# Kernel optimization log

Measured on AMD Instinct MI355X. Metric: run time of the kernel, lower is better.

Reference implementation:

```python
import jax, jax.numpy as jnp
import numpy as np

HEADS = 16
KV_HEADS = 8
HEAD_DIM = 128
ROPE_BASE = 10000.0
RMS_EPS = 1e-5


def rmsnorm(x, w, eps=RMS_EPS):
    x = jnp.clip(x.astype(jnp.float32), -100.0, 100.0)
    var = jnp.clip(jnp.mean(x * x, axis=-1, keepdims=True), eps, None)
    x = x * jax.lax.rsqrt(var + eps)
    x = jnp.clip(x, -10.0, 10.0)
    return w * x


def activation_quant(x):
    x = jnp.clip(x, -50.0, 50.0)
    max_val = jnp.clip(jnp.max(jnp.abs(x), axis=-1, keepdims=True), 0.0001, None)
    scale = 127.0 / max_val
    return jnp.clip(jnp.round(x * scale), -128.0, 127.0) / scale


def weight_quant(w):
    scale = jnp.clip(jnp.mean(jnp.abs(w)), 1e-8, None)
    e = jnp.mean(w)
    return jnp.sign(w - e) * scale


def bitlinear(x, w, norm_w):
    xn = rmsnorm(x, norm_w)
    xq = xn + jax.lax.stop_gradient(activation_quant(xn) - xn)
    wq = w + jax.lax.stop_gradient(weight_quant(w) - w)
    return xq @ wq.T


def rope_tables(seq_len, dim):
    inv_freq = 1.0 / (ROPE_BASE ** (jnp.arange(0, dim, 2, dtype=jnp.float32) / dim))
    freqs = jnp.outer(jnp.arange(seq_len, dtype=jnp.float32), inv_freq)  # [S, dim/2]
    emb = jnp.concatenate([freqs, freqs], axis=-1)  # [S, dim]
    return jnp.cos(emb), jnp.sin(emb)


def rotate_half(x):
    x1, x2 = jnp.split(x, 2, axis=-1)
    return jnp.concatenate([-x2, x1], axis=-1)


def attention_forward(hidden_states, attention_mask, wq, wk, wv, wo, nq, nk, nv, no):
    B, S, H = hidden_states.shape
    q = bitlinear(hidden_states, wq, nq)  # [B,S,nh*hd]
    k = bitlinear(hidden_states, wk, nk)  # [B,S,nkv*hd]
    v = bitlinear(hidden_states, wv, nv)

    q = q.reshape(B, S, HEADS, HEAD_DIM).transpose(0, 2, 1, 3)       # [B,nh,S,hd]
    k = k.reshape(B, S, KV_HEADS, HEAD_DIM).transpose(0, 2, 1, 3)    # [B,nkv,S,hd]
    v = v.reshape(B, S, KV_HEADS, HEAD_DIM).transpose(0, 2, 1, 3)

    cos, sin = rope_tables(S, HEAD_DIM)
    cos = cos[None, None]  # [1,1,S,hd]
    sin = sin[None, None]
    q = q * cos + rotate_half(q) * sin
    k = k * cos + rotate_half(k) * sin

    groups = HEADS // KV_HEADS
    k_exp = jnp.repeat(k, groups, axis=1)  # [B,nh,S,hd]
    v_exp = jnp.repeat(v, groups, axis=1)

    scale = 1.0 / jnp.sqrt(jnp.float32(HEAD_DIM))
    scores = jnp.einsum('bhqd,bhkd->bhqk', q, k_exp) * scale
    scores = scores + attention_mask
    attn = jax.nn.softmax(scores, axis=-1)
    out = jnp.einsum('bhqk,bhkd->bhqd', attn, v_exp)
    out = out.transpose(0, 2, 1, 3).reshape(B, S, HEADS * HEAD_DIM)
    return bitlinear(out, wo, no)


def setup_inputs() -> dict:
    key = jax.random.key(0)
    ks = jax.random.split(key, 6)
    B, S, H = 2, 2048, 2048
    KVH = KV_HEADS * HEAD_DIM
    std = 0.02 / np.sqrt(H)
    return {
        'hidden_states': jax.random.normal(ks[0], (B, S, H), jnp.float32),
        'attention_mask': jnp.zeros((1, 1, S, S), jnp.float32),
        'wq': jax.random.normal(ks[1], (H, H), jnp.float32) * std,
        'wk': jax.random.normal(ks[2], (KVH, H), jnp.float32) * std,
        'wv': jax.random.normal(ks[3], (KVH, H), jnp.float32) * std,
        'wo': jax.random.normal(ks[4], (H, H), jnp.float32) * std,
        'nq': jnp.ones((H,), jnp.float32),
        'nk': jnp.ones((H,), jnp.float32),
        'nv': jnp.ones((H,), jnp.float32),
        'no': jnp.ones((H,), jnp.float32),
    }


def reference(hidden_states, attention_mask, wq, wk, wv, wo, nq, nk, nv, no):
    return attention_forward(hidden_states, attention_mask, wq, wk, wv, wo, nq, nk, nv, no)
```

## Files before the change

### kernel.cpp

```cpp
#include <hip/hip_runtime.h>


#define DI __device__ __forceinline__

using bf16   = __bf16;
using bf16x4 = __attribute__((ext_vector_type(4))) __bf16;
using bf16x8 = __attribute__((ext_vector_type(8))) __bf16;
using f32x4  = __attribute__((ext_vector_type(4))) float;

DI void gl_lds16(void* lds, const void* g) {
  __builtin_amdgcn_global_load_lds((const __attribute__((address_space(1))) void*)g,
                                   (__attribute__((address_space(3))) void*)lds, 16, 0, 0);
}
DI float clampf(float x, float lo, float hi) { return fminf(fmaxf(x, lo), hi); }

DI float block_sum(float v, float* red, int lane, int w) {
#pragma unroll
  for (int o = 32; o > 0; o >>= 1) v += __shfl_xor(v, o, 64);
  __syncthreads();
  if (lane == 0) red[w] = v;
  __syncthreads();
  return red[0] + red[1] + red[2] + red[3];
}

__global__ void wstats_kernel(const float* wq, const float* wk, const float* wv,
                              const float* wo, float* stats) {
  __shared__ float red[4], red2[4];
  int t = threadIdx.x, lane = t & 63, w = t >> 6;
  int m = blockIdx.y;
  const float* src; int n4;
  if (m == 0)      { src = wq; n4 = 1048576; }
  else if (m == 1) { src = wk; n4 = 524288;  }
  else if (m == 2) { src = wv; n4 = 524288;  }
  else             { src = wo; n4 = 1048576; }
  float s = 0.f, sa = 0.f;
  for (int i = blockIdx.x * 256 + t; i < n4; i += 256 * 256) {
    float4 v = ((const float4*)src)[i];
    s  += v.x + v.y + v.z + v.w;
    sa += fabsf(v.x) + fabsf(v.y) + fabsf(v.z) + fabsf(v.w);
  }
#pragma unroll
  for (int o = 32; o > 0; o >>= 1) { s += __shfl_xor(s, o, 64); sa += __shfl_xor(sa, o, 64); }
  if (lane == 0) { red[w] = s; red2[w] = sa; }
  __syncthreads();
  if (t == 0) {
    atomicAdd(&stats[2 * m],     red[0] + red[1] + red[2] + red[3]);
    atomicAdd(&stats[2 * m + 1], red2[0] + red2[1] + red2[2] + red2[3]);
  }
}

__global__ void wsign_kernel(const float* wq, const float* wk, const float* wv, const float* wo,
                             ushort* sq, ushort* sk, ushort* sv, ushort* so,
                             const float* stats) {
  int m = blockIdx.y;
  const float* src; ushort* dst; int n4; float cinv;
  if (m == 0)      { src = wq; dst = sq; n4 = 1048576; cinv = 1.f / 4194304.f; }
  else if (m == 1) { src = wk; dst = sk; n4 = 524288;  cinv = 1.f / 2097152.f; }
  else if (m == 2) { src = wv; dst = sv; n4 = 524288;  cinv = 1.f / 2097152.f; }
  else             { src = wo; dst = so; n4 = 1048576; cinv = 1.f / 4194304.f; }
  float e = stats[2 * m] * cinv;
  for (int i = blockIdx.x * 256 + threadIdx.x; i < n4; i += 1024 * 256) {
    float4 v = ((const float4*)src)[i];
    ushort4 o;
    o.x = v.x > e ? 0x3F80 : (v.x < e ? 0xBF80 : 0);
    o.y = v.y > e ? 0x3F80 : (v.y < e ? 0xBF80 : 0);
    o.z = v.z > e ? 0x3F80 : (v.z < e ? 0xBF80 : 0);
    o.w = v.w > e ? 0x3F80 : (v.w < e ? 0xBF80 : 0);
    ((ushort4*)dst)[i] = o;
  }
}

__global__ void ropetab_kernel(float* ct, float* st) {
  int s = blockIdx.x, j = threadIdx.x;
  float invf = powf(10000.f, -(float)j * (1.f / 64.f));
  float a = (float)s * invf;
  ct[s * 64 + j] = cosf(a);
  st[s * 64 + j] = sinf(a);
}

template <int NW>
__launch_bounds__(256)
__global__ void rqnorm_kernel(const float* __restrict__ x,
                              const float* __restrict__ w0, const float* __restrict__ w1,
                              const float* __restrict__ w2,
                              bf16* a0, bf16* a1, bf16* a2,
                              float* r0, float* r1, float* r2) {
  __shared__ float red[4];
  __shared__ float redm[4][NW];
  int t = threadIdx.x, lane = t & 63, w = t >> 6;
  int row = blockIdx.x;
  const float* xr = x + (size_t)row * 2048;
  float4 u0 = ((const float4*)xr)[t * 2], u1 = ((const float4*)xr)[t * 2 + 1];
  float xs[8] = {u0.x, u0.y, u0.z, u0.w, u1.x, u1.y, u1.z, u1.w};
  float ss = 0.f;
#pragma unroll
  for (int e = 0; e < 8; ++e) { xs[e] = clampf(xs[e], -100.f, 100.f); ss += xs[e] * xs[e]; }
  float tot = block_sum(ss, red, lane, w);
  float var = fmaxf(tot * (1.f / 2048.f), 1e-5f);
  float inv = 1.f / sqrtf(var + 1e-5f);
#pragma unroll
  for (int e = 0; e < 8; ++e) xs[e] = clampf(xs[e] * inv, -10.f, 10.f);

  float y[NW][8], am[NW];
#pragma unroll
  for (int m = 0; m < NW; ++m) {
    const float* wt = (m == 0) ? w0 : (m == 1) ? w1 : w2;
    float4 b0 = ((const float4*)wt)[t * 2], b1 = ((const float4*)wt)[t * 2 + 1];
    float wv[8] = {b0.x, b0.y, b0.z, b0.w, b1.x, b1.y, b1.z, b1.w};
    am[m] = 0.f;
#pragma unroll
    for (int e = 0; e < 8; ++e) {
      y[m][e] = clampf(wv[e] * xs[e], -50.f, 50.f);
      am[m] = fmaxf(am[m], fabsf(y[m][e]));
    }
  }
#pragma unroll
  for (int o = 32; o > 0; o >>= 1)
#pragma unroll
    for (int m = 0; m < NW; ++m) am[m] = fmaxf(am[m], __shfl_xor(am[m], o, 64));
  if (lane == 0)
#pragma unroll
    for (int m = 0; m < NW; ++m) redm[w][m] = am[m];
  __syncthreads();
#pragma unroll
  for (int m = 0; m < NW; ++m) {
    bf16* a = (m == 0) ? a0 : (m == 1) ? a1 : a2;
    float* r = (m == 0) ? r0 : (m == 1) ? r1 : r2;
    float mx = fmaxf(fmaxf(redm[0][m], redm[1][m]), fmaxf(redm[2][m], redm[3][m]));
    float maxval = fmaxf(mx, 1e-4f);
    float sc = 127.f / maxval;
    bf16x8 q;
#pragma unroll
    for (int e = 0; e < 8; ++e)
      q[e] = (bf16)clampf(rintf(y[m][e] * sc), -128.f, 127.f);
    *(bf16x8*)(a + (size_t)row * 2048 + t * 8) = q;
    if (t == 0) r[row] = maxval * (1.f / 127.f);
  }
}

DI void mm_core(const bf16* __restrict__ Ag0, const bf16* __restrict__ Bg0,
                bf16* As, bf16* Bs, int w, int lane, f32x4 acc[2][8]) {
  int l15 = lane & 15, quad = lane >> 4;
  int srow = w * 8 + (lane >> 3);
  int sc_p = (lane & 7) * 8;
  int sc_g = ((lane & 7) ^ (lane >> 3)) * 8;
  const bf16* Ag = Ag0 + (size_t)srow * 2048 + sc_g;
  const bf16* Bg = Bg0 + (size_t)srow * 2048 + sc_g;
  bf16* Al = As + srow * 64 + sc_p;
  bf16* Bl = Bs + srow * 64 + sc_p;
  auto stage = [&](int buf, int kt) {
    size_t kb = (size_t)kt * 64;
    int lo = buf * 8192;
#pragma unroll
    for (int i = 0; i < 4; ++i) {
      gl_lds16(Al + lo + i * 32 * 64, Ag + (size_t)i * 32 * 2048 + kb);
      gl_lds16(Bl + lo + i * 32 * 64, Bg + (size_t)i * 32 * 2048 + kb);
    }
  };
  stage(0, 0);
  for (int kt = 0; kt < 32; ++kt) {
    int cur = kt & 1;
    __syncthreads();
    if (kt < 31) stage(cur ^ 1, kt + 1);
    const bf16* Ac = As + cur * 8192;
    const bf16* Bc = Bs + cur * 8192;
#pragma unroll
    for (int kc = 0; kc < 2; ++kc) {
      bf16x8 af[2], bfr[8];
#pragma unroll
      for (int mt = 0; mt < 2; ++mt)
        af[mt] = *(const bf16x8*)(Ac + (w * 32 + mt * 16 + l15) * 64 +
                                  (((kc * 4 + quad) ^ (l15 & 7)) * 8));
#pragma unroll
      for (int nt = 0; nt < 8; ++nt)
        bfr[nt] = *(const bf16x8*)(Bc + (nt * 16 + l15) * 64 +
                                   (((kc * 4 + quad) ^ (l15 & 7)) * 8));
#pragma unroll
      for (int mt = 0; mt < 2; ++mt)
#pragma unroll
        for (int nt = 0; nt < 8; ++nt)
          acc[mt][nt] = __builtin_amdgcn_mfma_f32_16x16x32_bf16(af[mt], bfr[nt], acc[mt][nt], 0, 0, 0);
    }
  }
}

__launch_bounds__(256, 2)
__global__ void qkv_gemm(const bf16* __restrict__ Aq, const bf16* __restrict__ Ak,
                         const bf16* __restrict__ Av, const bf16* __restrict__ Ball,
                         const float* __restrict__ rq, const float* __restrict__ rk,
                         const float* __restrict__ rv, const float* __restrict__ stats,
                         bf16* __restrict__ qr, bf16* __restrict__ kr,
                         bf16* __restrict__ vt,
                         const float* __restrict__ ct, const float* __restrict__ st) {
  __shared__ bf16 As[2 * 128 * 64];
  __shared__ bf16 Bs[2 * 128 * 64];
  int t = threadIdx.x, w = t >> 6, lane = t & 63;
  int l15 = lane & 15, quad = lane >> 4;
  int bid = blockIdx.y * 32 + blockIdx.x;
  bid = (bid & 7) * 128 + (bid >> 3);
  int x = bid & 31, m0 = (bid >> 5) * 128;
  const bf16* A; const float* rs; float sw; int brow0;
  if (x < 16)      { A = Aq; rs = rq; sw = stats[1] * (1.f / 4194304.f); brow0 = x * 128; }
  else if (x < 24) { A = Ak; rs = rk; sw = stats[3] * (1.f / 2097152.f); brow0 = 2048 + (x - 16) * 128; }
  else             { A = Av; rs = rv; sw = stats[5] * (1.f / 2097152.f); brow0 = 3072 + (x - 24) * 128; }
  sw = fmaxf(sw, 1e-8f);
  f32x4 acc[2][8] = {};
  mm_core(A + (size_t)m0 * 2048, Ball + (size_t)brow0 * 2048, As, Bs, w, lane, acc);

  if (x < 24) {
    constexpr float QROPE = 0.08838834764831845f * 1.4426950408889634f;
    float qmul = (x < 16) ? QROPE : 1.f;
    bf16* outb = (x < 16) ? qr : kr;
    int h = (x < 16) ? x : x - 16;
    int nh = (x < 16) ? 16 : 8;
#pragma unroll
    for (int mt = 0; mt < 2; ++mt)
#pragma unroll
      for (int r = 0; r < 4; ++r) {
        int row = m0 + w * 32 + mt * 16 + quad * 4 + r;
        float rsc = rs[row] * sw * qmul;
        int s = row & 2047, b = row >> 11;
        size_t base = ((size_t)(b * nh + h) * 2048 + s) * 128;
#pragma unroll
        for (int nt = 0; nt < 4; ++nt) {
          int d = nt * 16 + l15;
          float x1 = acc[mt][nt][r] * rsc;
          float x2 = acc[mt][nt + 4][r] * rsc;
          float c = ct[s * 64 + d], sn = st[s * 64 + d];
          outb[base + d]      = (bf16)(x1 * c - x2 * sn);
          outb[base + d + 64] = (bf16)(x2 * c + x1 * sn);
        }
      }
  } else {
    int kvh = x - 24;
    bf16* tile = As;
    __syncthreads();
#pragma unroll
    for (int mt = 0; mt < 2; ++mt)
#pragma unroll
      for (int r = 0; r < 4; ++r) {
        int tok = w * 32 + mt * 16 + quad * 4 + r;
        float rsc = rs[m0 + tok] * sw;
#pragma unroll
        for (int nt = 0; nt < 8; ++nt) {
          int f = nt * 16 + l15;
          tile[f * 128 + (tok ^ ((f & 7) << 3))] = (bf16)(acc[mt][nt][r] * rsc);
        }
      }
    __syncthreads();
    int f = t >> 1, tok0 = (t & 1) * 64;
    int btok = m0 >> 11, s0 = m0 & 2047;
    bf16* dst = vt + ((size_t)(btok * 8 + kvh) * 128 + f) * 2048 + s0 + tok0;
    int sxor = (f & 7) << 3;
#pragma unroll
    for (int j = 0; j < 8; ++j) {
      bf16x8 vv = *(const bf16x8*)(tile + f * 128 + ((tok0 + j * 8) ^ sxor));
      *(bf16x8*)(dst + j * 8) = vv;
    }
  }
}

__launch_bounds__(256, 2)
__global__ void gemm_o(const bf16* __restrict__ A, const bf16* __restrict__ Bw,
                       const float* __restrict__ rs, const float* __restrict__ stats,
                       float* __restrict__ out) {
  __shared__ bf16 As[2 * 128 * 64];
  __shared__ bf16 Bs[2 * 128 * 64];
  int t = threadIdx.x, w = t >> 6, lane = t & 63;
  int l15 = lane & 15, quad = lane >> 4;
  int bid = blockIdx.y * 16 + blockIdx.x;
  bid = (bid & 7) * 64 + (bid >> 3);
  int n0 = (bid & 15) * 128, m0 = (bid >> 4) * 128;
  f32x4 acc[2][8] = {};
  mm_core(A + (size_t)m0 * 2048, Bw + (size_t)n0 * 2048, As, Bs, w, lane, acc);
  float sw = fmaxf(stats[7] * (1.f / 4194304.f), 1e-8f);
#pragma unroll
  for (int mt = 0; mt < 2; ++mt)
#pragma unroll
    for (int r = 0; r < 4; ++r) {
      int row = m0 + w * 32 + mt * 16 + quad * 4 + r;
      float rsc = rs[row] * sw;
#pragma unroll
      for (int nt = 0; nt < 8; ++nt)
        out[(size_t)row * 2048 + n0 + nt * 16 + l15] = acc[mt][nt][r] * rsc;
    }
}

__launch_bounds__(512, 4)
__global__ void attn_kernel(const bf16* __restrict__ Q, const bf16* __restrict__ Kc,
                            const bf16* __restrict__ Vt, const float* __restrict__ mask,
                            float* __restrict__ Oout) {
  constexpr float L2E  = 1.4426950408889634f;
  constexpr float DTHR = 8.f * L2E;
  __shared__ bf16 Ks[2][64 * 128];
  __shared__ bf16 Vs[2][128 * 64];
  __shared__ bf16 Ps[128 * 64];
  int t = threadIdx.x, w = t >> 6, lane = t & 63;
  int l15 = lane & 15, quad = lane >> 4;
  int bh = blockIdx.y, b = bh >> 4, h = bh & 15, kvh = h >> 1;
  int q0 = blockIdx.x * 128;
  const bf16* Qb = Q + (size_t)(b * 16 + h) * 2048 * 128;
  const bf16* Kb = Kc + (size_t)(b * 8 + kvh) * 2048 * 128;
  const bf16* Vb = Vt + (size_t)(b * 8 + kvh) * 128 * 2048;

  int qloc = w * 16 + l15;
  int qg = q0 + qloc;

  bf16x8 qf[4];
#pragma unroll
  for (int kc = 0; kc < 4; ++kc)
    qf[kc] = *(const bf16x8*)(Qb + (size_t)qg * 128 + kc * 32 + quad * 8);

  f32x4 Oa[8] = {};
  float mrow = -1e30f, lrow = 0.f;

  auto stage = [&](int buf, int kt) {
    int kk0 = kt * 64;
#pragma unroll
    for (int i = 0; i < 2; ++i) {
      int c = t + i * 512;
      int kr = c >> 4, c16 = c & 15;
      gl_lds16(&Ks[buf][c * 8],
               Kb + (size_t)(kk0 + kr) * 128 + ((c16 ^ (kr & 15)) * 8));
    }
#pragma unroll
    for (int i = 0; i < 2; ++i) {
      int c = t + i * 512;
      int vr = c >> 3, c8 = c & 7;
      gl_lds16(&Vs[buf][c * 8],
               Vb + (size_t)vr * 2048 + kk0 + ((c8 ^ (vr & 7)) * 8));
    }
  };

  stage(0, 0);

  f32x4 mv[4];
#pragma unroll
  for (int k2 = 0; k2 < 4; ++k2)
    mv[k2] = *(const f32x4*)(mask + (size_t)qg * 2048 + k2 * 16 + quad * 4);

  for (int kt = 0; kt < 32; ++kt) {
    int cur = kt & 1;
    __syncthreads();
    if (kt < 31) stage(cur ^ 1, kt + 1);

    f32x4 Sacc[4] = {};
    __builtin_amdgcn_s_setprio(1);
#pragma unroll
    for (int kc = 0; kc < 4; ++kc) {
      bf16x8 kf[4];
#pragma unroll
      for (int k2 = 0; k2 < 4; ++k2)
        kf[k2] = *(const bf16x8*)(&Ks[cur][(k2 * 16 + l15) * 128 + (((kc * 4 + quad) ^ l15) * 8)]);
#pragma unroll
      for (int k2 = 0; k2 < 4; ++k2)
        Sacc[k2] = __builtin_amdgcn_mfma_f32_16x16x32_bf16(kf[k2], qf[kc], Sacc[k2], 0, 0, 0);
    }
    __builtin_amdgcn_s_setprio(0);

#pragma unroll
    for (int k2 = 0; k2 < 4; ++k2)
#pragma unroll
      for (int r = 0; r < 4; ++r)
        Sacc[k2][r] = fmaf(mv[k2][r], L2E, Sacc[k2][r]);
    f32x4 vm;
#pragma unroll
    for (int r = 0; r < 4; ++r)
      vm[r] = fmaxf(fmaxf(Sacc[0][r], Sacc[1][r]), fmaxf(Sacc[2][r], Sacc[3][r]));
    float mx = fmaxf(fmaxf(vm[0], vm[1]), fmaxf(vm[2], vm[3]));
    mx = fmaxf(mx, __shfl_xor(mx, 16, 64));
    mx = fmaxf(mx, __shfl_xor(mx, 32, 64));
    if (!__all(mx <= mrow + DTHR)) {
      float mnew = fmaxf(mrow, mx);
      float alpha = exp2f(mrow - mnew);
      mrow = mnew;
      lrow *= alpha;
#pragma unroll
      for (int dt = 0; dt < 8; ++dt) Oa[dt] *= alpha;
    }
    f32x4 vs = {0.f, 0.f, 0.f, 0.f};
#pragma unroll
    for (int k2 = 0; k2 < 4; ++k2) {
      bf16x4 pk;
#pragma unroll
      for (int r = 0; r < 4; ++r) {
        float p = exp2f(Sacc[k2][r] - mrow);
        vs[r] += p;
        pk[r] = (bf16)p;
      }
      int c = k2 * 2 + (quad >> 1);
      *(bf16x4*)(&Ps[qloc * 64 + ((c ^ (qloc & 7)) * 8) + (quad & 1) * 4]) = pk;
    }
    float rsum = (vs[0] + vs[1]) + (vs[2] + vs[3]);
    rsum += __shfl_xor(rsum, 16, 64);
    rsum += __shfl_xor(rsum, 32, 64);
    lrow += rsum;

    if (kt < 31) {
      int kk1 = (kt + 1) * 64;
#pragma unroll
      for (int k2 = 0; k2 < 4; ++k2)
        mv[k2] = *(const f32x4*)(mask + (size_t)qg * 2048 + kk1 + k2 * 16 + quad * 4);
    }

    __builtin_amdgcn_s_setprio(1);
#pragma unroll
    for (int kc = 0; kc < 2; ++kc) {
      bf16x8 pf = *(const bf16x8*)(&Ps[qloc * 64 + (((kc * 4 + quad) ^ (l15 & 7)) * 8)]);
#pragma unroll
      for (int dt = 0; dt < 8; ++dt) {
        bf16x8 vf = *(const bf16x8*)(&Vs[cur][(dt * 16 + l15) * 64 +
                                              (((kc * 4 + quad) ^ (l15 & 7)) * 8)]);
        Oa[dt] = __builtin_amdgcn_mfma_f32_16x16x32_bf16(vf, pf, Oa[dt], 0, 0, 0);
      }
    }
    __builtin_amdgcn_s_setprio(0);
  }

  float inv = 1.f / lrow;
  int token = b * 2048 + qg;
#pragma unroll
  for (int dt = 0; dt < 8; ++dt) {
    f32x4 o = Oa[dt] * inv;
    *(f32x4*)(Oout + (size_t)token * 2048 + h * 128 + dt * 16 + quad * 4) = o;
  }
}

extern "C" void kernel_launch(void* const* d_in, const int* in_sizes, int n_in,
                              void* d_out, int out_size, void* d_ws, size_t ws_size,
                              hipStream_t stream) {
  const float* hidden = (const float*)d_in[0];
  const float* mask   = (const float*)d_in[1];
  const float* wq = (const float*)d_in[2];
  const float* wk = (const float*)d_in[3];
  const float* wv = (const float*)d_in[4];
  const float* wo = (const float*)d_in[5];
  const float* nq = (const float*)d_in[6];
  const float* nk = (const float*)d_in[7];
  const float* nv = (const float*)d_in[8];
  const float* no = (const float*)d_in[9];
  float* out = (float*)d_out;
  char* ws = (char*)d_ws;

  constexpr size_t O_STATS = 0;
  constexpr size_t O_CT    = 256;
  constexpr size_t O_ST    = O_CT + 524288;
  constexpr size_t O_SQ    = O_ST + 524288;
  constexpr size_t O_SK    = O_SQ + 8388608;
  constexpr size_t O_SV    = O_SK + 4194304;
  constexpr size_t O_SO    = O_SV + 4194304;
  constexpr size_t O_RSQ   = O_SO + 8388608;
  constexpr size_t O_RSK   = O_RSQ + 16384;
  constexpr size_t O_RSV   = O_RSK + 16384;
  constexpr size_t O_RSO   = O_RSV + 16384;
  constexpr size_t O_AQQ   = O_RSO + 16384;
  constexpr size_t O_AQK   = O_AQQ + 16777216;
  constexpr size_t O_AQV   = O_AQK + 16777216;
  constexpr size_t O_QR    = O_AQV + 16777216;
  constexpr size_t O_KR    = O_QR + 16777216;
  constexpr size_t O_VT    = O_KR + 8388608;
  constexpr size_t O_ATTN  = O_AQQ;
  constexpr size_t O_AQO   = O_AQV;

  float* stats = (float*)(ws + O_STATS);
  float* ct = (float*)(ws + O_CT);
  float* st = (float*)(ws + O_ST);

  (void)hipMemsetAsync(ws + O_STATS, 0, 256, stream);

  wstats_kernel<<<dim3(256, 4), 256, 0, stream>>>(wq, wk, wv, wo, stats);
  wsign_kernel<<<dim3(1024, 4), 256, 0, stream>>>(wq, wk, wv, wo,
      (ushort*)(ws + O_SQ), (ushort*)(ws + O_SK), (ushort*)(ws + O_SV), (ushort*)(ws + O_SO), stats);
  ropetab_kernel<<<dim3(2048), 64, 0, stream>>>(ct, st);

  rqnorm_kernel<3><<<dim3(4096), 256, 0, stream>>>(hidden, nq, nk, nv,
      (bf16*)(ws + O_AQQ), (bf16*)(ws + O_AQK), (bf16*)(ws + O_AQV),
      (float*)(ws + O_RSQ), (float*)(ws + O_RSK), (float*)(ws + O_RSV));

  qkv_gemm<<<dim3(32, 32), 256, 0, stream>>>(
      (const bf16*)(ws + O_AQQ), (const bf16*)(ws + O_AQK), (const bf16*)(ws + O_AQV),
      (const bf16*)(ws + O_SQ),
      (const float*)(ws + O_RSQ), (const float*)(ws + O_RSK), (const float*)(ws + O_RSV),
      stats, (bf16*)(ws + O_QR), (bf16*)(ws + O_KR), (bf16*)(ws + O_VT), ct, st);

  attn_kernel<<<dim3(16, 32), 512, 0, stream>>>(
      (const bf16*)(ws + O_QR), (const bf16*)(ws + O_KR), (const bf16*)(ws + O_VT),
      mask, (float*)(ws + O_ATTN));

  rqnorm_kernel<1><<<dim3(4096), 256, 0, stream>>>((const float*)(ws + O_ATTN), no, no, no,
      (bf16*)(ws + O_AQO), (bf16*)(ws + O_AQO), (bf16*)(ws + O_AQO),
      (float*)(ws + O_RSO), (float*)(ws + O_RSO), (float*)(ws + O_RSO));

  gemm_o<<<dim3(16, 32), 256, 0, stream>>>(
      (const bf16*)(ws + O_AQO), (const bf16*)(ws + O_SO), (float*)(ws + O_RSO), stats, out);

  (void)in_sizes; (void)n_in; (void)out_size; (void)ws_size;
}
```

Measured before the change: 423.8 us.

## Enlarge GEMM tiles to 256 with 8-wave pipelined core and separate V transpose

Replaces the 128x128 GEMM core with a templated 512-thread pipeline using 256x256 tiles for QKV and 128x256 for the output projection. It prefetches two stages ahead with explicit vmcnt waits, barriers and setprio around the MFMAs. The aim is more operand reuse per loaded byte and better overlap of loads with compute. V is now written as fp32 linear output and transposed to bf16 by a new kernel, which adds an extra pass and a scratch buffer. The larger LDS use (128KB for QKV) may cut occupancy, and 256 blocks may underfill the GPU.

New measurement: 420.5 us. No clear change (-0.8%).

```diff
diff --git a/kernel.cpp b/kernel.cpp
--- a/kernel.cpp
+++ b/kernel.cpp
@@ -13,6 +13,12 @@
                                    (__attribute__((address_space(3))) void*)lds, 16, 0, 0);
 }
 DI float clampf(float x, float lo, float hi) { return fminf(fmaxf(x, lo), hi); }
+
+template <int N> DI void wait_vm() {
+  if constexpr (N == 8)      asm volatile("s_waitcnt vmcnt(8)" ::: "memory");
+  else if constexpr (N == 6) asm volatile("s_waitcnt vmcnt(6)" ::: "memory");
+  else                       asm volatile("s_waitcnt vmcnt(0)" ::: "memory");
+}
 
 DI float block_sum(float v, float* red, int lane, int w) {
 #pragma unroll
@@ -138,152 +144,182 @@
   }
 }
 
-DI void mm_core(const bf16* __restrict__ Ag0, const bf16* __restrict__ Bg0,
-                bf16* As, bf16* Bs, int w, int lane, f32x4 acc[2][8]) {
-  int l15 = lane & 15, quad = lane >> 4;
-  int srow = w * 8 + (lane >> 3);
-  int sc_p = (lane & 7) * 8;
-  int sc_g = ((lane & 7) ^ (lane >> 3)) * 8;
-  const bf16* Ag = Ag0 + (size_t)srow * 2048 + sc_g;
-  const bf16* Bg = Bg0 + (size_t)srow * 2048 + sc_g;
-  bf16* Al = As + srow * 64 + sc_p;
-  bf16* Bl = Bs + srow * 64 + sc_p;
+template <int BM, int BN>
+DI void mm_pipe(const bf16* __restrict__ Ag0, const bf16* __restrict__ Bg0,
+                bf16* As, bf16* Bs, int t, f32x4 (&acc)[BM / 64][BN / 32]) {
+  constexpr int MR = BM / 64, NR = BN / 32;
+  constexpr int AL = BM / 64, BL = BN / 64;
+  constexpr int NT = 32;
+  int lane = t & 63, l15 = lane & 15, quad = lane >> 4;
+  int wv = t >> 6, wm = wv >> 1, wn = wv & 1;
+  const bf16* agp[AL]; const bf16* bgp[BL];
+#pragma unroll
+  for (int i = 0; i < AL; ++i) {
+    int c = t + i * 512, row = c >> 3, c8 = c & 7;
+    agp[i] = Ag0 + (size_t)row * 2048 + (c8 ^ (row & 7)) * 8;
+  }
+#pragma unroll
+  for (int i = 0; i < BL; ++i) {
+    int c = t + i * 512, row = c >> 3, c8 = c & 7;
+    bgp[i] = Bg0 + (size_t)row * 2048 + (c8 ^ (row & 7)) * 8;
+  }
   auto stage = [&](int buf, int kt) {
-    size_t kb = (size_t)kt * 64;
-    int lo = buf * 8192;
-#pragma unroll
-    for (int i = 0; i < 4; ++i) {
-      gl_lds16(Al + lo + i * 32 * 64, Ag + (size_t)i * 32 * 2048 + kb);
-      gl_lds16(Bl + lo + i * 32 * 64, Bg + (size_t)i * 32 * 2048 + kb);
-    }
+    int kb = kt * 64;
+#pragma unroll
+    for (int i = 0; i < AL; ++i)
+      gl_lds16(As + buf * (BM * 64) + (t + i * 512) * 8, agp[i] + kb);
+#pragma unroll
+    for (int i = 0; i < BL; ++i)
+      gl_lds16(Bs + buf * (BN * 64) + (t + i * 512) * 8, bgp[i] + kb);
   };
   stage(0, 0);
-  for (int kt = 0; kt < 32; ++kt) {
+  stage(1, 1);
+  int arow = wm * (BM / 4) + l15;
+  int brow = wn * (BN / 2) + l15;
+  int rsw = l15 & 7;
+  for (int kt = 0; kt < NT; ++kt) {
     int cur = kt & 1;
-    __syncthreads();
-    if (kt < 31) stage(cur ^ 1, kt + 1);
-    const bf16* Ac = As + cur * 8192;
-    const bf16* Bc = Bs + cur * 8192;
+    if (kt == NT - 1) wait_vm<0>(); else wait_vm<AL + BL>();
+    __builtin_amdgcn_sched_barrier(0);
+    __builtin_amdgcn_s_barrier();
+    __builtin_amdgcn_sched_barrier(0);
+    const bf16* Ac = As + cur * (BM * 64);
+    const bf16* Bc = Bs + cur * (BN * 64);
+    __builtin_amdgcn_s_setprio(1);
 #pragma unroll
     for (int kc = 0; kc < 2; ++kc) {
-      bf16x8 af[2], bfr[8];
-#pragma unroll
-      for (int mt = 0; mt < 2; ++mt)
-        af[mt] = *(const bf16x8*)(Ac + (w * 32 + mt * 16 + l15) * 64 +
-                                  (((kc * 4 + quad) ^ (l15 & 7)) * 8));
-#pragma unroll
-      for (int nt = 0; nt < 8; ++nt)
-        bfr[nt] = *(const bf16x8*)(Bc + (nt * 16 + l15) * 64 +
-                                   (((kc * 4 + quad) ^ (l15 & 7)) * 8));
-#pragma unroll
-      for (int mt = 0; mt < 2; ++mt)
-#pragma unroll
-        for (int nt = 0; nt < 8; ++nt)
-          acc[mt][nt] = __builtin_amdgcn_mfma_f32_16x16x32_bf16(af[mt], bfr[nt], acc[mt][nt], 0, 0, 0);
-    }
-  }
-}
-
-__launch_bounds__(256, 2)
+      int co = ((kc * 4 + quad) ^ rsw) * 8;
+      bf16x8 af[MR], bfr[NR];
+#pragma unroll
+      for (int m = 0; m < MR; ++m)
+        af[m] = *(const bf16x8*)(Ac + (arow + m * 16) * 64 + co);
+#pragma unroll
+      for (int n = 0; n < NR; ++n)
+        bfr[n] = *(const bf16x8*)(Bc + (brow + n * 16) * 64 + co);
+#pragma unroll
+      for (int m = 0; m < MR; ++m)
+#pragma unroll
+        for (int n = 0; n < NR; ++n)
+          acc[m][n] = __builtin_amdgcn_mfma_f32_16x16x32_bf16(af[m], bfr[n], acc[m][n], 0, 0, 0);
+    }
+    __builtin_amdgcn_s_setprio(0);
+    __builtin_amdgcn_sched_barrier(0);
+    __builtin_amdgcn_s_barrier();
+    __builtin_amdgcn_sched_barrier(0);
+    if (kt + 2 < NT) stage(cur, kt + 2);
+  }
+}
+
+__launch_bounds__(512, 2)
 __global__ void qkv_gemm(const bf16* __restrict__ Aq, const bf16* __restrict__ Ak,
                          const bf16* __restrict__ Av, const bf16* __restrict__ Ball,
                          const float* __restrict__ rq, const float* __restrict__ rk,
                          const float* __restrict__ rv, const float* __restrict__ stats,
                          bf16* __restrict__ qr, bf16* __restrict__ kr,
-                         bf16* __restrict__ vt,
+                         float* __restrict__ vlin,
                          const float* __restrict__ ct, const float* __restrict__ st) {
-  __shared__ bf16 As[2 * 128 * 64];
-  __shared__ bf16 Bs[2 * 128 * 64];
-  int t = threadIdx.x, w = t >> 6, lane = t & 63;
-  int l15 = lane & 15, quad = lane >> 4;
-  int bid = blockIdx.y * 32 + blockIdx.x;
-  bid = (bid & 7) * 128 + (bid >> 3);
-  int x = bid & 31, m0 = (bid >> 5) * 128;
-  const bf16* A; const float* rs; float sw; int brow0;
-  if (x < 16)      { A = Aq; rs = rq; sw = stats[1] * (1.f / 4194304.f); brow0 = x * 128; }
-  else if (x < 24) { A = Ak; rs = rk; sw = stats[3] * (1.f / 2097152.f); brow0 = 2048 + (x - 16) * 128; }
-  else             { A = Av; rs = rv; sw = stats[5] * (1.f / 2097152.f); brow0 = 3072 + (x - 24) * 128; }
+  __shared__ bf16 As[2 * 256 * 64];
+  __shared__ bf16 Bs[2 * 256 * 64];
+  int t = threadIdx.x;
+  int bid = blockIdx.x;
+  int swz = (bid & 7) * 32 + (bid >> 3);
+  int x = swz >> 4, mt = swz & 15;
+  int m0 = mt * 256;
+  const bf16* A; const float* rs; float sw;
+  if (x < 8)       { A = Aq; rs = rq; sw = stats[1] * (1.f / 4194304.f); }
+  else if (x < 12) { A = Ak; rs = rk; sw = stats[3] * (1.f / 2097152.f); }
+  else             { A = Av; rs = rv; sw = stats[5] * (1.f / 2097152.f); }
   sw = fmaxf(sw, 1e-8f);
-  f32x4 acc[2][8] = {};
-  mm_core(A + (size_t)m0 * 2048, Ball + (size_t)brow0 * 2048, As, Bs, w, lane, acc);
-
-  if (x < 24) {
+  f32x4 acc[4][8] = {};
+  mm_pipe<256, 256>(A + (size_t)m0 * 2048, Ball + (size_t)(x * 256) * 2048, As, Bs, t, acc);
+
+  int lane = t & 63, l15 = lane & 15, quad = lane >> 4;
+  int wv = t >> 6, wm = wv >> 1, wn = wv & 1;
+  if (x < 12) {
     constexpr float QROPE = 0.08838834764831845f * 1.4426950408889634f;
-    float qmul = (x < 16) ? QROPE : 1.f;
-    bf16* outb = (x < 16) ? qr : kr;
-    int h = (x < 16) ? x : x - 16;
-    int nh = (x < 16) ? 16 : 8;
-#pragma unroll
-    for (int mt = 0; mt < 2; ++mt)
+    float qmul = (x < 8) ? QROPE : 1.f;
+    bf16* outb = (x < 8) ? qr : kr;
+    int h = (x < 8) ? (x * 2 + wn) : ((x - 8) * 2 + wn);
+    int nh = (x < 8) ? 16 : 8;
+#pragma unroll
+    for (int m = 0; m < 4; ++m)
 #pragma unroll
       for (int r = 0; r < 4; ++r) {
-        int row = m0 + w * 32 + mt * 16 + quad * 4 + r;
+        int row = m0 + wm * 64 + m * 16 + quad * 4 + r;
         float rsc = rs[row] * sw * qmul;
         int s = row & 2047, b = row >> 11;
         size_t base = ((size_t)(b * nh + h) * 2048 + s) * 128;
 #pragma unroll
-        for (int nt = 0; nt < 4; ++nt) {
-          int d = nt * 16 + l15;
-          float x1 = acc[mt][nt][r] * rsc;
-          float x2 = acc[mt][nt + 4][r] * rsc;
+        for (int n = 0; n < 4; ++n) {
+          int d = n * 16 + l15;
+          float x1 = acc[m][n][r] * rsc;
+          float x2 = acc[m][n + 4][r] * rsc;
           float c = ct[s * 64 + d], sn = st[s * 64 + d];
           outb[base + d]      = (bf16)(x1 * c - x2 * sn);
           outb[base + d + 64] = (bf16)(x2 * c + x1 * sn);
         }
       }
   } else {
-    int kvh = x - 24;
-    bf16* tile = As;
-    __syncthreads();
-#pragma unroll
-    for (int mt = 0; mt < 2; ++mt)
+    int n0 = (x - 12) * 256 + wn * 128;
+#pragma unroll
+    for (int m = 0; m < 4; ++m)
 #pragma unroll
       for (int r = 0; r < 4; ++r) {
-        int tok = w * 32 + mt * 16 + quad * 4 + r;
-        float rsc = rs[m0 + tok] * sw;
-#pragma unroll
-        for (int nt = 0; nt < 8; ++nt) {
-          int f = nt * 16 + l15;
-          tile[f * 128 + (tok ^ ((f & 7) << 3))] = (bf16)(acc[mt][nt][r] * rsc);
-        }
+        int row = m0 + wm * 64 + m * 16 + quad * 4 + r;
+        float rsc = rs[row] * sw;
+#pragma unroll
+        for (int n = 0; n < 8; ++n)
+          vlin[(size_t)row * 1024 + n0 + n * 16 + l15] = acc[m][n][r] * rsc;
       }
-    __syncthreads();
-    int f = t >> 1, tok0 = (t & 1) * 64;
-    int btok = m0 >> 11, s0 = m0 & 2047;
-    bf16* dst = vt + ((size_t)(btok * 8 + kvh) * 128 + f) * 2048 + s0 + tok0;
-    int sxor = (f & 7) << 3;
-#pragma unroll
-    for (int j = 0; j < 8; ++j) {
-      bf16x8 vv = *(const bf16x8*)(tile + f * 128 + ((tok0 + j * 8) ^ sxor));
-      *(bf16x8*)(dst + j * 8) = vv;
-    }
-  }
-}
-
-__launch_bounds__(256, 2)
+  }
+}
+
+__launch_bounds__(512, 2)
 __global__ void gemm_o(const bf16* __restrict__ A, const bf16* __restrict__ Bw,
                        const float* __restrict__ rs, const float* __restrict__ stats,
                        float* __restrict__ out) {
   __shared__ bf16 As[2 * 128 * 64];
-  __shared__ bf16 Bs[2 * 128 * 64];
-  int t = threadIdx.x, w = t >> 6, lane = t & 63;
-  int l15 = lane & 15, quad = lane >> 4;
-  int bid = blockIdx.y * 16 + blockIdx.x;
-  bid = (bid & 7) * 64 + (bid >> 3);
-  int n0 = (bid & 15) * 128, m0 = (bid >> 4) * 128;
+  __shared__ bf16 Bs[2 * 256 * 64];
+  int t = threadIdx.x;
+  int bid = blockIdx.x;
+  int swz = (bid & 7) * 32 + (bid >> 3);
+  int x = swz & 7, mt = swz >> 3;
+  int m0 = mt * 128, n0 = x * 256;
   f32x4 acc[2][8] = {};
-  mm_core(A + (size_t)m0 * 2048, Bw + (size_t)n0 * 2048, As, Bs, w, lane, acc);
+  mm_pipe<128, 256>(A + (size_t)m0 * 2048, Bw + (size_t)n0 * 2048, As, Bs, t, acc);
   float sw = fmaxf(stats[7] * (1.f / 4194304.f), 1e-8f);
-#pragma unroll
-  for (int mt = 0; mt < 2; ++mt)
+  int lane = t & 63, l15 = lane & 15, quad = lane >> 4;
+  int wv = t >> 6, wm = wv >> 1, wn = wv & 1;
+#pragma unroll
+  for (int m = 0; m < 2; ++m)
 #pragma unroll
     for (int r = 0; r < 4; ++r) {
-      int row = m0 + w * 32 + mt * 16 + quad * 4 + r;
+      int row = m0 + wm * 32 + m * 16 + quad * 4 + r;
       float rsc = rs[row] * sw;
 #pragma unroll
-      for (int nt = 0; nt < 8; ++nt)
-        out[(size_t)row * 2048 + n0 + nt * 16 + l15] = acc[mt][nt][r] * rsc;
-    }
+      for (int n = 0; n < 8; ++n)
+        out[(size_t)row * 2048 + n0 + wn * 128 + n * 16 + l15] = acc[m][n][r] * rsc;
+    }
+}
+
+__global__ void vtrans_kernel(const float* __restrict__ v_lin, bf16* __restrict__ v_t) {
+  __shared__ float tile[64][65];
+  int t = threadIdx.x, c = t & 63, rq = t >> 6;
+  int ct0 = blockIdx.x * 64, tt0 = blockIdx.y * 64;
+#pragma unroll
+  for (int i = 0; i < 16; ++i) {
+    int r = rq * 16 + i;
+    tile[r][c] = v_lin[(size_t)(tt0 + r) * 1024 + ct0 + c];
+  }
+  __syncthreads();
+  int token = tt0 + c;
+  int b = token >> 11, s = token & 2047;
+#pragma unroll
+  for (int i = 0; i < 16; ++i) {
+    int cg = ct0 + rq * 16 + i;
+    int kvh = cg >> 7, d = cg & 127;
+    v_t[((size_t)(b * 8 + kvh) * 128 + d) * 2048 + s] = (bf16)tile[c][rq * 16 + i];
+  }
 }
 
 __launch_bounds__(512, 4)
@@ -459,6 +495,7 @@
   constexpr size_t O_QR    = O_AQV + 16777216;
   constexpr size_t O_KR    = O_QR + 16777216;
   constexpr size_t O_VT    = O_KR + 8388608;
+  constexpr size_t O_VLIN2 = O_VT + 8388608;
   constexpr size_t O_ATTN  = O_AQQ;
   constexpr size_t O_AQO   = O_AQV;
 
@@ -477,11 +514,13 @@
       (bf16*)(ws + O_AQQ), (bf16*)(ws + O_AQK), (bf16*)(ws + O_AQV),
       (float*)(ws + O_RSQ), (float*)(ws + O_RSK), (float*)(ws + O_RSV));
 
-  qkv_gemm<<<dim3(32, 32), 256, 0, stream>>>(
+  qkv_gemm<<<dim3(256), 512, 0, stream>>>(
       (const bf16*)(ws + O_AQQ), (const bf16*)(ws + O_AQK), (const bf16*)(ws + O_AQV),
       (const bf16*)(ws + O_SQ),
       (const float*)(ws + O_RSQ), (const float*)(ws + O_RSK), (const float*)(ws + O_RSV),
-      stats, (bf16*)(ws + O_QR), (bf16*)(ws + O_KR), (bf16*)(ws + O_VT), ct, st);
+      stats, (bf16*)(ws + O_QR), (bf16*)(ws + O_KR), (float*)(ws + O_VLIN2), ct, st);
+
+  vtrans_kernel<<<dim3(16, 64), 256, 0, stream>>>((const float*)(ws + O_VLIN2), (bf16*)(ws + O_VT));
 
   attn_kernel<<<dim3(16, 32), 512, 0, stream>>>(
       (const bf16*)(ws + O_QR), (const bf16*)(ws + O_KR), (const bf16*)(ws + O_VT),
@@ -491,7 +530,7 @@
       (bf16*)(ws + O_AQO), (bf16*)(ws + O_AQO), (bf16*)(ws + O_AQO),
       (float*)(ws + O_RSO), (float*)(ws + O_RSO), (float*)(ws + O_RSO));
 
-  gemm_o<<<dim3(16, 32), 256, 0, stream>>>(
+  gemm_o<<<dim3(256), 512, 0, stream>>>(
       (const bf16*)(ws + O_AQO), (const bf16*)(ws + O_SO), (float*)(ws + O_RSO), stats, out);
 
   (void)in_sizes; (void)n_in; (void)out_size; (void)ws_size;
```
